# Performance work log

Measured on AMD Instinct MI355X. Metric: run time of the kernel, lower is better.

## Reference

```python
import jax, jax.numpy as jnp
import numpy as np

B, S, D = 8, 2048, 512  # batch, seq_len, d_model (= units*heads = 64*8)


def setup_inputs() -> dict:
    key = jax.random.key(0)
    k1, k2, k3, k4 = jax.random.split(key, 4)
    scale = 1.0 / np.sqrt(D)
    return {
        "data": jax.random.normal(k1, (B, S, D), dtype=jnp.float32),
        "Wq": jax.random.normal(k2, (D, D), dtype=jnp.float32) * scale,
        "Wk": jax.random.normal(k3, (D, D), dtype=jnp.float32) * scale,
        "Wv": jax.random.normal(k4, (D, D), dtype=jnp.float32) * scale,
    }


def reference(data, Wq, Wk, Wv):
    # Bias-free projections (no head split in the original module).
    q = data @ Wq  # [B,S,D]
    k = data @ Wk
    v = data @ Wv
    scores = jnp.einsum("bsd,btd->bst", q, k)  # [B,S,S]
    # NOTE: original scales by sqrt(weight.shape[-1]) == sqrt(seq_len), not sqrt(d_k).
    scores = scores / jnp.sqrt(jnp.float32(scores.shape[-1]))
    # Causal mask: (w + 1e6) * tril - 1e6  ==  where(tril, w, -1e6)
    causal = jnp.tril(jnp.ones((scores.shape[1], scores.shape[2]), dtype=bool))
    scores = jnp.where(causal[None, :, :], scores, jnp.float32(-1e6))
    attn = jax.nn.softmax(scores, axis=-1)
    return jnp.einsum("bst,btd->bsd", attn, v)  # [B,S,D]
```

## Files before the change

kernel.cpp:

```cpp
#include <hip/hip_runtime.h>

typedef unsigned short u16;
typedef __attribute__((ext_vector_type(8))) short short8;
typedef __attribute__((ext_vector_type(4))) float f32x4;


__device__ __forceinline__ u16 f2bf(float f) {
    unsigned u = __float_as_uint(f);
    u += 0x7fffu + ((u >> 16) & 1u);
    return (u16)(u >> 16);
}

__device__ __forceinline__ void lds_cp16(const u16* g, u16* l) {
#if defined(__has_builtin) && __has_builtin(__builtin_amdgcn_global_load_lds)
    __builtin_amdgcn_global_load_lds(
        (const __attribute__((address_space(1))) void*)g,
        (__attribute__((address_space(3))) void*)l, 16, 0, 0);
#else
    *(uint4*)l = *(const uint4*)g;
#endif
}

template <int MI, bool ROWSUM>
__device__ __forceinline__ void gemm64(const u16* __restrict__ Ag, int lda,
                                       const u16* __restrict__ Bg, int ldb,
                                       int ksteps, u16* Alds, u16* Blds,
                                       f32x4 (&acc)[MI][4], f32x4* accL) {
    const int t = threadIdx.x;
    const int lane = t & 63, w = t >> 6;
    const int l15 = lane & 15, g4 = lane >> 4;
    const int wr = (w >> 1) * (MI * 16);
    const int wc = (w & 1) * 64;
    const int swz = l15 & 7;
    const short ob = (short)0x3f80;
    const short8 ones = {ob, ob, ob, ob, ob, ob, ob, ob};

    for (int kt = 0; kt < ksteps; ++kt) {
        __syncthreads();
#pragma unroll
        for (int p = 0; p < MI; ++p) {
            const int gi = t + p * 256;
            const int row = gi >> 3;
            const int gl = (gi & 7) ^ (row & 7);
            lds_cp16(Ag + (size_t)row * lda + kt * 64 + gl * 8, Alds + gi * 8);
        }
#pragma unroll
        for (int p = 0; p < 4; ++p) {
            const int gi = t + p * 256;
            const int row = gi >> 3;
            const int gl = (gi & 7) ^ (row & 7);
            lds_cp16(Bg + (size_t)row * ldb + kt * 64 + gl * 8, Blds + gi * 8);
        }
        __syncthreads();
#pragma unroll
        for (int ks = 0; ks < 2; ++ks) {
            short8 a[MI], b[4];
#pragma unroll
            for (int i = 0; i < MI; ++i) {
                const int r = wr + i * 16 + l15;
                a[i] = *(const short8*)(Alds + r * 64 + (((ks * 4 + g4) ^ swz) * 8));
            }
#pragma unroll
            for (int j = 0; j < 4; ++j) {
                const int r = wc + j * 16 + l15;
                b[j] = *(const short8*)(Blds + r * 64 + (((ks * 4 + g4) ^ swz) * 8));
            }
#pragma unroll
            for (int i = 0; i < MI; ++i)
#pragma unroll
                for (int j = 0; j < 4; ++j)
                    acc[i][j] = __builtin_amdgcn_mfma_f32_16x16x32_bf16(a[i], b[j], acc[i][j], 0, 0, 0);
            if constexpr (ROWSUM) {
#pragma unroll
                for (int i = 0; i < MI; ++i)
                    accL[i] = __builtin_amdgcn_mfma_f32_16x16x32_bf16(a[i], ones, accL[i], 0, 0, 0);
            }
        }
    }
}


__global__ void k_cvt(const float4* __restrict__ X4, ushort4* __restrict__ Xb4,
                      const float* __restrict__ Wq, const float* __restrict__ Wk,
                      const float* __restrict__ Wv, u16* __restrict__ Wt) {
    const int bid = blockIdx.x, t = threadIdx.x;
    if (bid < 2048) {
        const int n4 = (8 * 2048 * 512) / 4;
        for (int i = bid * 256 + t; i < n4; i += 2048 * 256) {
            float4 v = X4[i];
            ushort4 o;
            o.x = f2bf(v.x); o.y = f2bf(v.y); o.z = f2bf(v.z); o.w = f2bf(v.w);
            Xb4[i] = o;
        }
    } else {
        const int e0 = ((bid - 2048) * 256 + t) * 4;
#pragma unroll
        for (int p = 0; p < 4; ++p) {
            const int idx = e0 + p;
            const int z = idx >> 18;
            const int rem = idx & 262143;
            float v;
            if (z == 0) v = Wq[rem];
            else if (z == 1) v = Wk[rem];
            else { int n = rem >> 9, k = rem & 511; v = Wv[k * 512 + n]; }
            Wt[idx] = f2bf(v);
        }
    }
}

__global__ __launch_bounds__(256, 4) void k_gemm_m(const u16* __restrict__ Wt, u16* __restrict__ Mt) {
    __shared__ alignas(16) u16 Alds[8192];
    __shared__ alignas(16) u16 Blds[8192];
    const int mt = blockIdx.x & 3, nt = blockIdx.x >> 2;
    const u16* Ag = Wt + 0 * 512 * 512 + (size_t)mt * 128 * 512;
    const u16* Bg = Wt + 1 * 512 * 512 + (size_t)nt * 128 * 512;
    f32x4 acc[4][4] = {};
    gemm64<4, false>(Ag, 512, Bg, 512, 8, Alds, Blds, acc, (f32x4*)nullptr);

    const int t = threadIdx.x, lane = t & 63, w = t >> 6;
    const int wr = (w >> 1) * 64, wc = (w & 1) * 64;
    const float sc = 0.022097086912079608f;
#pragma unroll
    for (int i = 0; i < 4; ++i)
#pragma unroll
        for (int j = 0; j < 4; ++j)
#pragma unroll
            for (int r = 0; r < 4; ++r) {
                int e = mt * 128 + wr + i * 16 + 4 * (lane >> 4) + r;
                int f = nt * 128 + wc + j * 16 + (lane & 15);
                Mt[(size_t)f * 512 + e] = f2bf(acc[i][j][r] * sc);
            }
}

__global__ __launch_bounds__(256, 4) void k_proj(const u16* __restrict__ Xb, const u16* __restrict__ Wt,
                                                 const u16* __restrict__ Mt,
                                                 u16* __restrict__ Gb, u16* __restrict__ Vt) {
    __shared__ alignas(16) u16 Alds[8192];
    __shared__ alignas(16) u16 Blds[8192];
    const int bid = blockIdx.x;
    const int u = bid >> 3;
    const int z = u >> 6;
    const int nt = (u >> 4) & 3;
    const int mt = (bid & 7) * 16 + (u & 15);
    const u16* Ag = Xb + (size_t)mt * 128 * 512;
    const u16* Bg = (z == 0) ? (Mt + (size_t)nt * 128 * 512)
                             : (Wt + 2 * 512 * 512 + (size_t)nt * 128 * 512);
    f32x4 acc[4][4] = {};
    gemm64<4, false>(Ag, 512, Bg, 512, 8, Alds, Blds, acc, (f32x4*)nullptr);

    const int t = threadIdx.x, lane = t & 63, w = t >> 6;
    const int wr = (w >> 1) * 64, wc = (w & 1) * 64;
    if (z == 0) {
#pragma unroll
        for (int i = 0; i < 4; ++i)
#pragma unroll
            for (int j = 0; j < 4; ++j)
#pragma unroll
                for (int r = 0; r < 4; ++r) {
                    int m = mt * 128 + wr + i * 16 + 4 * (lane >> 4) + r;
                    int n = nt * 128 + wc + j * 16 + (lane & 15);
                    Gb[(size_t)m * 512 + n] = f2bf(acc[i][j][r]);
                }
    } else {
        int b = mt >> 4;
#pragma unroll
        for (int i = 0; i < 4; ++i)
#pragma unroll
            for (int j = 0; j < 4; ++j) {
                int s0 = (mt * 128 + wr + i * 16 + 4 * (lane >> 4)) & 2047;
                int d = nt * 128 + wc + j * 16 + (lane & 15);
                ushort4 pk;
                pk.x = f2bf(acc[i][j][0]); pk.y = f2bf(acc[i][j][1]);
                pk.z = f2bf(acc[i][j][2]); pk.w = f2bf(acc[i][j][3]);
                *(ushort4*)(Vt + (size_t)b * 512 * 2048 + (size_t)d * 2048 + s0) = pk;
            }
    }
}

__global__ __launch_bounds__(256, 4) void k_scores(const u16* __restrict__ Gb, const u16* __restrict__ Xb,
                                                   u16* __restrict__ P) {
    const int bid = blockIdx.x;
    const int bz = bid & 7;
    const int tt = bid >> 3;
    int qi = (int)((sqrtf(8.0f * tt + 1.0f) - 1.0f) * 0.5f);
    while ((qi + 1) * (qi + 2) / 2 <= tt) ++qi;
    while (qi * (qi + 1) / 2 > tt) --qi;
    const int kvj = tt - qi * (qi + 1) / 2;

    __shared__ alignas(16) u16 Alds[8192];
    __shared__ alignas(16) u16 Blds[8192];
    const u16* Ag = Gb + (size_t)bz * 2048 * 512 + (size_t)qi * 128 * 512;
    const u16* Bg = Xb + (size_t)bz * 2048 * 512 + (size_t)kvj * 128 * 512;
    f32x4 acc[4][4] = {};
    gemm64<4, false>(Ag, 512, Bg, 512, 8, Alds, Blds, acc, (f32x4*)nullptr);

    const int t = threadIdx.x, lane = t & 63, w = t >> 6;
    const int wr = (w >> 1) * 64, wc = (w & 1) * 64;
    u16* Pb = P + (size_t)bz * 2048 * 2048;
#pragma unroll
    for (int i = 0; i < 4; ++i)
#pragma unroll
        for (int j = 0; j < 4; ++j)
#pragma unroll
            for (int r = 0; r < 4; ++r) {
                int q = qi * 128 + wr + i * 16 + 4 * (lane >> 4) + r;
                int kv = kvj * 128 + wc + j * 16 + (lane & 15);
                float pv = (kv <= q) ? __expf(acc[i][j][r]) : 0.0f;
                Pb[(size_t)q * 2048 + kv] = f2bf(pv);
            }
}

__global__ __launch_bounds__(256, 4) void k_pv(const u16* __restrict__ P, const u16* __restrict__ Vt,
                                               float* __restrict__ Out) {
    __shared__ alignas(16) u16 Alds[4096];
    __shared__ alignas(16) u16 Blds[8192];
    const int bid = blockIdx.x;
    const int bz = bid & 7;
    const int u = bid >> 3;
    const int g = u >> 5;
    const int s = u & 31;
    const int nt = g;
    const int qi2 = (g & 1) ? (31 - s) : s;
    const int ksteps = qi2 + 1;

    const u16* Ag = P + (size_t)bz * 2048 * 2048 + (size_t)qi2 * 64 * 2048;
    const u16* Bg = Vt + (size_t)bz * 512 * 2048 + (size_t)nt * 128 * 2048;
    f32x4 acc[2][4] = {};
    f32x4 accL[2] = {};
    gemm64<2, true>(Ag, 2048, Bg, 2048, ksteps, Alds, Blds, acc, accL);

    const int t = threadIdx.x, lane = t & 63, w = t >> 6;
    const int l = lane & 15, g4 = lane >> 4;
    const int wr = (w >> 1) * 32, wc = (w & 1) * 64;
#pragma unroll
    for (int i = 0; i < 2; ++i) {
        float inv[4];
#pragma unroll
        for (int r = 0; r < 4; ++r) inv[r] = 1.0f / accL[i][r];
#pragma unroll
        for (int j = 0; j < 4; ++j) {
            const int d = nt * 128 + wc + j * 16 + l;
#pragma unroll
            for (int r = 0; r < 4; ++r) {
                const int q = qi2 * 64 + wr + i * 16 + 4 * g4 + r;
                Out[(size_t)bz * 2048 * 512 + (size_t)q * 512 + d] = acc[i][j][r] * inv[r];
            }
        }
    }
}


extern "C" void kernel_launch(void* const* d_in, const int* in_sizes, int n_in,
                              void* d_out, int out_size, void* d_ws, size_t ws_size,
                              hipStream_t stream) {
    const float* data = (const float*)d_in[0];
    const float* Wq = (const float*)d_in[1];
    const float* Wk = (const float*)d_in[2];
    const float* Wv = (const float*)d_in[3];
    float* out = (float*)d_out;
    char* ws = (char*)d_ws;

    u16* Xb = (u16*)(ws);
    u16* Gb = (u16*)(ws + 16777216);
    u16* Mt = (u16*)(ws + 33554432);
    u16* Vt = (u16*)(ws + 50331648);
    u16* Wt = (u16*)(ws + 67108864);
    u16* P  = (u16*)(ws + 68681728);

    k_cvt<<<2816, 256, 0, stream>>>((const float4*)data, (ushort4*)Xb, Wq, Wk, Wv, Wt);
    k_gemm_m<<<16, 256, 0, stream>>>(Wt, Mt);
    k_proj<<<1024, 256, 0, stream>>>(Xb, Wt, Mt, Gb, Vt);
    k_scores<<<1088, 256, 0, stream>>>(Gb, Xb, P);
    k_pv<<<1024, 256, 0, stream>>>(P, Vt, out);
}
```

Before: 111.7 us.

## Double-buffer GEMM mainloop with async LDS loads and k-step of 32

Adds a gemm32p routine that splits K into 32-wide steps and double-buffers the A/B tiles in LDS. The global_load_lds for step s+2 is issued while MFMAs for step s run, with explicit vmcnt waits and raw barriers. It replaces the single-buffered 64-wide loop in the projection, scores and PV kernels. The aim is to hide global memory latency behind compute, at the cost of twice as many barriers and per-step overhead. It also relies on hand-tuned waitcnt counts that must match the number of loads issued.

```diff
diff --git a/kernel.cpp b/kernel.cpp
--- a/kernel.cpp
+++ b/kernel.cpp
@@ -19,6 +19,12 @@
 #else
     *(uint4*)l = *(const uint4*)g;
 #endif
+}
+
+__device__ __forceinline__ void bar() {
+    asm volatile("" ::: "memory");
+    __builtin_amdgcn_s_barrier();
+    asm volatile("" ::: "memory");
 }
 
 template <int MI, bool ROWSUM>
@@ -75,6 +81,78 @@
                 for (int i = 0; i < MI; ++i)
                     accL[i] = __builtin_amdgcn_mfma_f32_16x16x32_bf16(a[i], ones, accL[i], 0, 0, 0);
             }
+        }
+    }
+}
+
+template <int MI, bool ROWSUM>
+__device__ __forceinline__ void gemm32p(const u16* __restrict__ Ag, int lda,
+                                        const u16* __restrict__ Bg, int ldb,
+                                        int S , u16* Alds, u16* Blds,
+                                        f32x4 (&acc)[MI][4], f32x4* accL) {
+    const int t = threadIdx.x;
+    const int lane = t & 63, w = t >> 6;
+    const int l15 = lane & 15, g4 = lane >> 4;
+    const int wr = (w >> 1) * (MI * 16);
+    const int wc = (w & 1) * 64;
+    const short ob = (short)0x3f80;
+    const short8 ones = {ob, ob, ob, ob, ob, ob, ob, ob};
+
+    auto stage = [&](int s, int buf) {
+#pragma unroll
+        for (int p = 0; p < MI / 2; ++p) {
+            const int gi = t + p * 256;
+            const int row = gi >> 2, pos = gi & 3;
+            const int gl = pos ^ ((row >> 1) & 3);
+            lds_cp16(Ag + (size_t)row * lda + s * 32 + gl * 8, Alds + buf * (MI * 1024) + gi * 8);
+        }
+#pragma unroll
+        for (int p = 0; p < 2; ++p) {
+            const int gi = t + p * 256;
+            const int row = gi >> 2, pos = gi & 3;
+            const int gl = pos ^ ((row >> 1) & 3);
+            lds_cp16(Bg + (size_t)row * ldb + s * 32 + gl * 8, Blds + buf * 4096 + gi * 8);
+        }
+    };
+
+    stage(0, 0);
+    if (S > 1) stage(1, 1);
+    for (int s = 0; s < S; ++s) {
+        const int cur = s & 1;
+        if (s + 1 < S) {
+            if constexpr (MI == 4) asm volatile("s_waitcnt vmcnt(4)" ::: "memory");
+            else                   asm volatile("s_waitcnt vmcnt(3)" ::: "memory");
+        } else {
+            asm volatile("s_waitcnt vmcnt(0)" ::: "memory");
+        }
+        bar();
+
+        short8 a[MI], b[4];
+#pragma unroll
+        for (int i = 0; i < MI; ++i) {
+            const int r = wr + i * 16 + l15;
+            a[i] = *(const short8*)(Alds + cur * (MI * 1024) + r * 32 + ((g4 ^ ((r >> 1) & 3)) << 3));
+        }
+#pragma unroll
+        for (int j = 0; j < 4; ++j) {
+            const int r = wc + j * 16 + l15;
+            b[j] = *(const short8*)(Blds + cur * 4096 + r * 32 + ((g4 ^ ((r >> 1) & 3)) << 3));
+        }
+        asm volatile("s_waitcnt lgkmcnt(0)" ::: "memory");
+        __builtin_amdgcn_sched_barrier(0);
+        bar();
+
+        if (s + 2 < S) stage(s + 2, cur);
+
+#pragma unroll
+        for (int i = 0; i < MI; ++i)
+#pragma unroll
+            for (int j = 0; j < 4; ++j)
+                acc[i][j] = __builtin_amdgcn_mfma_f32_16x16x32_bf16(a[i], b[j], acc[i][j], 0, 0, 0);
+        if constexpr (ROWSUM) {
+#pragma unroll
+            for (int i = 0; i < MI; ++i)
+                accL[i] = __builtin_amdgcn_mfma_f32_16x16x32_bf16(a[i], ones, accL[i], 0, 0, 0);
         }
     }
 }
@@ -146,7 +224,7 @@
     const u16* Bg = (z == 0) ? (Mt + (size_t)nt * 128 * 512)
                              : (Wt + 2 * 512 * 512 + (size_t)nt * 128 * 512);
     f32x4 acc[4][4] = {};
-    gemm64<4, false>(Ag, 512, Bg, 512, 8, Alds, Blds, acc, (f32x4*)nullptr);
+    gemm32p<4, false>(Ag, 512, Bg, 512, 16, Alds, Blds, acc, (f32x4*)nullptr);
 
     const int t = threadIdx.x, lane = t & 63, w = t >> 6;
     const int wr = (w >> 1) * 64, wc = (w & 1) * 64;
@@ -192,7 +270,7 @@
     const u16* Ag = Gb + (size_t)bz * 2048 * 512 + (size_t)qi * 128 * 512;
     const u16* Bg = Xb + (size_t)bz * 2048 * 512 + (size_t)kvj * 128 * 512;
     f32x4 acc[4][4] = {};
-    gemm64<4, false>(Ag, 512, Bg, 512, 8, Alds, Blds, acc, (f32x4*)nullptr);
+    gemm32p<4, false>(Ag, 512, Bg, 512, 16, Alds, Blds, acc, (f32x4*)nullptr);
 
     const int t = threadIdx.x, lane = t & 63, w = t >> 6;
     const int wr = (w >> 1) * 64, wc = (w & 1) * 64;
@@ -221,13 +299,13 @@
     const int s = u & 31;
     const int nt = g;
     const int qi2 = (g & 1) ? (31 - s) : s;
-    const int ksteps = qi2 + 1;
+    const int S = (qi2 + 1) * 2;
 
     const u16* Ag = P + (size_t)bz * 2048 * 2048 + (size_t)qi2 * 64 * 2048;
     const u16* Bg = Vt + (size_t)bz * 512 * 2048 + (size_t)nt * 128 * 2048;
     f32x4 acc[2][4] = {};
     f32x4 accL[2] = {};
-    gemm64<2, true>(Ag, 2048, Bg, 2048, ksteps, Alds, Blds, acc, accL);
+    gemm32p<2, true>(Ag, 2048, Bg, 2048, S, Alds, Blds, acc, accL);
 
     const int t = threadIdx.x, lane = t & 63, w = t >> 6;
     const int l = lane & 15, g4 = lane >> 4;
```

Result: slower. 118.2 us (+5.7%).

## Fuse Wq·Wkᵀ weight-product GEMM into the conversion kernel, dropping a launch

Applied to the files above, without the earlier changes.

The separate k_gemm_m kernel, which multiplied the bf16-converted Wq and Wk to form the scaled Mt matrix, is removed. Sixteen extra blocks in k_cvt now compute that product directly from the fp32 weights, converting to bf16 in registers and issuing MFMA without LDS staging. Only Wv is still transposed and converted into Wt, and k_proj's V-projection pointer is adjusted to match. This saves a kernel launch and a serial dependency, but the 16 GEMM blocks read fp32 globals uncached through LDS and could become a long tail of the conversion kernel.

```diff
diff --git a/kernel.cpp b/kernel.cpp
--- a/kernel.cpp
+++ b/kernel.cpp
@@ -82,7 +82,8 @@
 
 __global__ void k_cvt(const float4* __restrict__ X4, ushort4* __restrict__ Xb4,
                       const float* __restrict__ Wq, const float* __restrict__ Wk,
-                      const float* __restrict__ Wv, u16* __restrict__ Wt) {
+                      const float* __restrict__ Wv, u16* __restrict__ Wt,
+                      u16* __restrict__ Mt) {
     const int bid = blockIdx.x, t = threadIdx.x;
     if (bid < 2048) {
         const int n4 = (8 * 2048 * 512) / 4;
@@ -92,44 +93,59 @@
             o.x = f2bf(v.x); o.y = f2bf(v.y); o.z = f2bf(v.z); o.w = f2bf(v.w);
             Xb4[i] = o;
         }
-    } else {
-        const int e0 = ((bid - 2048) * 256 + t) * 4;
+    } else if (bid < 2304) {
+        const int e0 = (bid - 2048) * 1024 + t * 4;
 #pragma unroll
         for (int p = 0; p < 4; ++p) {
             const int idx = e0 + p;
-            const int z = idx >> 18;
-            const int rem = idx & 262143;
-            float v;
-            if (z == 0) v = Wq[rem];
-            else if (z == 1) v = Wk[rem];
-            else { int n = rem >> 9, k = rem & 511; v = Wv[k * 512 + n]; }
-            Wt[idx] = f2bf(v);
-        }
-    }
-}
-
-__global__ __launch_bounds__(256, 4) void k_gemm_m(const u16* __restrict__ Wt, u16* __restrict__ Mt) {
-    __shared__ alignas(16) u16 Alds[8192];
-    __shared__ alignas(16) u16 Blds[8192];
-    const int mt = blockIdx.x & 3, nt = blockIdx.x >> 2;
-    const u16* Ag = Wt + 0 * 512 * 512 + (size_t)mt * 128 * 512;
-    const u16* Bg = Wt + 1 * 512 * 512 + (size_t)nt * 128 * 512;
-    f32x4 acc[4][4] = {};
-    gemm64<4, false>(Ag, 512, Bg, 512, 8, Alds, Blds, acc, (f32x4*)nullptr);
-
-    const int t = threadIdx.x, lane = t & 63, w = t >> 6;
-    const int wr = (w >> 1) * 64, wc = (w & 1) * 64;
-    const float sc = 0.022097086912079608f;
-#pragma unroll
-    for (int i = 0; i < 4; ++i)
-#pragma unroll
-        for (int j = 0; j < 4; ++j)
-#pragma unroll
-            for (int r = 0; r < 4; ++r) {
-                int e = mt * 128 + wr + i * 16 + 4 * (lane >> 4) + r;
-                int f = nt * 128 + wc + j * 16 + (lane & 15);
-                Mt[(size_t)f * 512 + e] = f2bf(acc[i][j][r] * sc);
-            }
+            const int n = idx >> 9, k = idx & 511;
+            Wt[idx] = f2bf(Wv[k * 512 + n]);
+        }
+    } else {
+        const int id = bid - 2304;
+        const int mt = id & 3, nt = id >> 2;
+        const int lane = t & 63, w = t >> 6;
+        const int l15 = lane & 15, g4 = lane >> 4;
+        const int wr = (w >> 1) * 64, wc = (w & 1) * 64;
+        const float* Ag = Wq + (size_t)mt * 128 * 512;
+        const float* Bg = Wk + (size_t)nt * 128 * 512;
+        f32x4 acc[4][4] = {};
+        for (int kt = 0; kt < 16; ++kt) {
+            short8 a[4], b[4];
+#pragma unroll
+            for (int i = 0; i < 4; ++i) {
+                const float* s = Ag + (size_t)(wr + i * 16 + l15) * 512 + kt * 32 + g4 * 8;
+                short8 v;
+#pragma unroll
+                for (int jj = 0; jj < 8; ++jj) v[jj] = (short)f2bf(s[jj]);
+                a[i] = v;
+            }
+#pragma unroll
+            for (int j = 0; j < 4; ++j) {
+                const float* s = Bg + (size_t)(wc + j * 16 + l15) * 512 + kt * 32 + g4 * 8;
+                short8 v;
+#pragma unroll
+                for (int jj = 0; jj < 8; ++jj) v[jj] = (short)f2bf(s[jj]);
+                b[j] = v;
+            }
+#pragma unroll
+            for (int i = 0; i < 4; ++i)
+#pragma unroll
+                for (int j = 0; j < 4; ++j)
+                    acc[i][j] = __builtin_amdgcn_mfma_f32_16x16x32_bf16(a[i], b[j], acc[i][j], 0, 0, 0);
+        }
+        const float sc = 0.022097086912079608f;
+#pragma unroll
+        for (int i = 0; i < 4; ++i)
+#pragma unroll
+            for (int j = 0; j < 4; ++j)
+#pragma unroll
+                for (int r = 0; r < 4; ++r) {
+                    int e = mt * 128 + wr + i * 16 + 4 * g4 + r;
+                    int f = nt * 128 + wc + j * 16 + l15;
+                    Mt[(size_t)f * 512 + e] = f2bf(acc[i][j][r] * sc);
+                }
+    }
 }
 
 __global__ __launch_bounds__(256, 4) void k_proj(const u16* __restrict__ Xb, const u16* __restrict__ Wt,
@@ -144,7 +160,7 @@
     const int mt = (bid & 7) * 16 + (u & 15);
     const u16* Ag = Xb + (size_t)mt * 128 * 512;
     const u16* Bg = (z == 0) ? (Mt + (size_t)nt * 128 * 512)
-                             : (Wt + 2 * 512 * 512 + (size_t)nt * 128 * 512);
+                             : (Wt + (size_t)nt * 128 * 512);
     f32x4 acc[4][4] = {};
     gemm64<4, false>(Ag, 512, Bg, 512, 8, Alds, Blds, acc, (f32x4*)nullptr);
 
@@ -267,8 +283,7 @@
     u16* Wt = (u16*)(ws + 67108864);
     u16* P  = (u16*)(ws + 68681728);
 
-    k_cvt<<<2816, 256, 0, stream>>>((const float4*)data, (ushort4*)Xb, Wq, Wk, Wv, Wt);
-    k_gemm_m<<<16, 256, 0, stream>>>(Wt, Mt);
+    k_cvt<<<2320, 256, 0, stream>>>((const float4*)data, (ushort4*)Xb, Wq, Wk, Wv, Wt, Mt);
     k_proj<<<1024, 256, 0, stream>>>(Xb, Wt, Mt, Gb, Vt);
     k_scores<<<1088, 256, 0, stream>>>(Gb, Xb, P);
     k_pv<<<1024, 256, 0, stream>>>(P, Vt, out);
```

After: 147.8 us. 1.32x slower.
